# Kernel tuning notes

Measured on AMD Instinct MI355X. Metric: run time of the kernel, lower is better.

Reference implementation:

```python
import jax, jax.numpy as jnp
import numpy as np

N_NODES = 50000
N_EDGES = 800000
D_IN, H, D_OUT = 128, 128, 64


def setup_inputs() -> dict:
    key = jax.random.key(0)
    ks = jax.random.split(key, 8)
    x = jax.random.normal(ks[0], (N_NODES, D_IN), dtype=jnp.float32)
    edge_index = jax.random.randint(ks[1], (2, N_EDGES), 0, N_NODES, dtype=jnp.int64)
    s = 0.05
    return {
        "x": x,
        "edge_index": edge_index,
        # PyG Linear weights are [out, in]; y = x @ W.T + b
        "W_rel1": jax.random.normal(ks[2], (H, D_IN), dtype=jnp.float32) * s,
        "W_root1": jax.random.normal(ks[3], (H, D_IN), dtype=jnp.float32) * s,
        "b1": jax.random.normal(ks[4], (H,), dtype=jnp.float32) * s,
        "W_rel2": jax.random.normal(ks[5], (D_OUT, H), dtype=jnp.float32) * s,
        "W_root2": jax.random.normal(ks[6], (D_OUT, H), dtype=jnp.float32) * s,
        "b2": jax.random.normal(ks[7], (D_OUT,), dtype=jnp.float32) * s,
    }


def graph_conv(x, src, dst, W_rel, W_root, b):
    # sum-aggregate raw neighbor features, then apply linear (equivalent to
    # transforming each message first, but cheaper: one gather + one GEMM).
    agg = jax.ops.segment_sum(x[src], dst, num_segments=N_NODES)  # [N, D]
    return jnp.einsum('nd,hd->nh', agg, W_rel) \
         + jnp.einsum('nd,hd->nh', x, W_root) + b


def reference(x, edge_index, W_rel1, W_root1, b1, W_rel2, W_root2, b2):
    src, dst = edge_index[0], edge_index[1]  # messages flow src -> dst
    t = jax.nn.relu(graph_conv(x, src, dst, W_rel1, W_root1, b1))
    t = graph_conv(t, src, dst, W_rel2, W_root2, b2)
    return t
```

## Files before the change

### kernel.cpp

```cpp
#include <hip/hip_runtime.h>

#define NNODES 50000
#define DIM 128
#define SCAN_CHUNK 4096
#define NSCAN 13
#define PREP_BLOCKS 3200
#define POISON ((int)0xAAAAAAAA)

typedef __attribute__((ext_vector_type(8))) __bf16 bf16x8;
typedef __attribute__((ext_vector_type(4))) float f32x4;

__device__ inline unsigned short f2b(float f) {
    unsigned int u = __float_as_uint(f);
    u += 0x7fffu + ((u >> 16) & 1u);
    return (unsigned short)(u >> 16);
}
__device__ inline float blo(unsigned int u) { return __uint_as_float(u << 16); }
__device__ inline float bhi(unsigned int u) { return __uint_as_float(u & 0xffff0000u); }
__device__ inline unsigned int pack2(float a, float b) {
    return (unsigned int)f2b(a) | ((unsigned int)f2b(b) << 16);
}

__global__ __launch_bounds__(256) void k_prep(
    const float* __restrict__ x, unsigned short* __restrict__ xb, int n4,
    const float* __restrict__ Wa1, const float* __restrict__ Wb1,
    const float* __restrict__ Wa2, const float* __restrict__ Wb2,
    unsigned short* __restrict__ wa1, unsigned short* __restrict__ wb1,
    unsigned short* __restrict__ wa2, unsigned short* __restrict__ wb2,
    const int* __restrict__ dst, int* __restrict__ counts,
    unsigned short* __restrict__ rank, int n_edges)
{
    const int gid = blockIdx.x * 256 + threadIdx.x;

    const int i1 = blockIdx.x * 512 + threadIdx.x;
    const int i2 = i1 + 256;
    const bool ok1 = i1 < n4, ok2 = i2 < n4;
    float4 v1, v2;
    if (ok1) v1 = reinterpret_cast<const float4*>(x)[i1];
    if (ok2) v2 = reinterpret_cast<const float4*>(x)[i2];

    if (gid < n_edges) {
        const int rep = threadIdx.x & 3;
        int rk = atomicAdd(&counts[rep * NNODES + dst[gid]], 1) - POISON;
        rank[gid] = (unsigned short)(rk | (rep << 14));
    }

    if (gid < 16384) { wa1[gid] = f2b(Wa1[gid]); wb1[gid] = f2b(Wb1[gid]); }
    if (gid < 8192)  { wa2[gid] = f2b(Wa2[gid]); wb2[gid] = f2b(Wb2[gid]); }

    if (ok1) {
        uint2 o;
        o.x = pack2(v1.x, v1.y);
        o.y = pack2(v1.z, v1.w);
        reinterpret_cast<uint2*>(xb)[i1] = o;
    }
    if (ok2) {
        uint2 o;
        o.x = pack2(v2.x, v2.y);
        o.y = pack2(v2.z, v2.w);
        reinterpret_cast<uint2*>(xb)[i2] = o;
    }
}

__global__ __launch_bounds__(1024) void k_scan_local(
    const int* __restrict__ counts, int* __restrict__ rowptr,
    int* __restrict__ bsum, uint2* __restrict__ repx2, int n)
{
    __shared__ int wsum[16];
    const int lane = threadIdx.x & 63;
    const int wid = threadIdx.x >> 6;
    int i = blockIdx.x * SCAN_CHUNK + threadIdx.x * 4;
    int4 v = make_int4(0, 0, 0, 0);
    if (i + 3 < n) {
        int4 c0 = *reinterpret_cast<const int4*>(counts + i);
        int4 c1 = *reinterpret_cast<const int4*>(counts + NNODES + i);
        int4 c2 = *reinterpret_cast<const int4*>(counts + 2 * NNODES + i);
        int4 c3 = *reinterpret_cast<const int4*>(counts + 3 * NNODES + i);
        c0.x -= POISON; c0.y -= POISON; c0.z -= POISON; c0.w -= POISON;
        c1.x -= POISON; c1.y -= POISON; c1.z -= POISON; c1.w -= POISON;
        c2.x -= POISON; c2.y -= POISON; c2.z -= POISON; c2.w -= POISON;
        c3.x -= POISON; c3.y -= POISON; c3.z -= POISON; c3.w -= POISON;
        v.x = c0.x + c1.x + c2.x + c3.x;
        v.y = c0.y + c1.y + c2.y + c3.y;
        v.z = c0.z + c1.z + c2.z + c3.z;
        v.w = c0.w + c1.w + c2.w + c3.w;
        uint2 r0, r1g, r2g, r3g;
        r0.x  = (unsigned)(c0.x) << 16;
        r0.y  = (unsigned)(c0.x + c1.x) | ((unsigned)(c0.x + c1.x + c2.x) << 16);
        r1g.x = (unsigned)(c0.y) << 16;
        r1g.y = (unsigned)(c0.y + c1.y) | ((unsigned)(c0.y + c1.y + c2.y) << 16);
        r2g.x = (unsigned)(c0.z) << 16;
        r2g.y = (unsigned)(c0.z + c1.z) | ((unsigned)(c0.z + c1.z + c2.z) << 16);
        r3g.x = (unsigned)(c0.w) << 16;
        r3g.y = (unsigned)(c0.w + c1.w) | ((unsigned)(c0.w + c1.w + c2.w) << 16);
        repx2[i + 0] = r0;
        repx2[i + 1] = r1g;
        repx2[i + 2] = r2g;
        repx2[i + 3] = r3g;
    } else {
#pragma unroll
        for (int j = 0; j < 3; ++j) {
            if (i + j < n) {
                int c0 = counts[i + j] - POISON;
                int c1 = counts[NNODES + i + j] - POISON;
                int c2 = counts[2 * NNODES + i + j] - POISON;
                int c3 = counts[3 * NNODES + i + j] - POISON;
                int t = c0 + c1 + c2 + c3;
                if (j == 0) v.x = t; else if (j == 1) v.y = t; else v.z = t;
                uint2 r;
                r.x = (unsigned)c0 << 16;
                r.y = (unsigned)(c0 + c1) | ((unsigned)(c0 + c1 + c2) << 16);
                repx2[i + j] = r;
            }
        }
    }
    int tot = v.x + v.y + v.z + v.w;
    int s = tot;
#pragma unroll
    for (int off = 1; off < 64; off <<= 1) {
        int t = __shfl_up(s, off);
        if (lane >= off) s += t;
    }
    if (lane == 63) wsum[wid] = s;
    __syncthreads();
    if (wid == 0 && lane < 16) {
        int ws = wsum[lane];
#pragma unroll
        for (int off = 1; off < 16; off <<= 1) {
            int t = __shfl_up(ws, off);
            if (lane >= off) ws += t;
        }
        wsum[lane] = ws;
    }
    __syncthreads();
    int prefix = ((wid > 0) ? wsum[wid - 1] : 0) + (s - tot);
    int4 o;
    o.x = prefix;
    o.y = prefix + v.x;
    o.z = o.y + v.y;
    o.w = o.z + v.z;
    if (i + 3 <= n) {
        *reinterpret_cast<int4*>(rowptr + i) = o;
    } else {
        if (i + 0 <= n) rowptr[i + 0] = o.x;
        if (i + 1 <= n) rowptr[i + 1] = o.y;
        if (i + 2 <= n) rowptr[i + 2] = o.z;
    }
    if (threadIdx.x == 1023) bsum[blockIdx.x] = wsum[15];
}

__device__ inline void build_prefix_lds(const int* __restrict__ bsum, int* pre) {
    if (threadIdx.x < 16) {
        int off = 0;
#pragma unroll 1
        for (int j = 0; j < NSCAN && j < (int)threadIdx.x; ++j) off += bsum[j];
        pre[threadIdx.x] = off;
    }
    __syncthreads();
}

__device__ inline int rep_off(uint2 rp, int r) {
    unsigned pw = (r & 2) ? rp.y : rp.x;
    return (r & 1) ? (int)(pw >> 16) : (int)(pw & 0xffffu);
}

__global__ __launch_bounds__(256) void k_place_gemm1(
    const int* __restrict__ src, const int* __restrict__ dst,
    const unsigned short* __restrict__ rank, const int* __restrict__ rowptr,
    const int* __restrict__ bsum, const uint2* __restrict__ repx2,
    unsigned short* __restrict__ srcs_sorted, int n_edges, int pblocks,
    const unsigned short* __restrict__ A,
    const unsigned short* __restrict__ Wu,
    const unsigned short* __restrict__ Wr,
    const float* __restrict__ bias,
    unsigned short* __restrict__ U,
    unsigned short* __restrict__ R,
    int n_nodes)
{
    if (blockIdx.x < (unsigned)pblocks) {
        __shared__ int pre[16];
        build_prefix_lds(bsum, pre);
        int e = ((int)blockIdx.x * 256 + threadIdx.x) * 8;
        if (e + 7 < n_edges) {
            int4 s4a = *reinterpret_cast<const int4*>(src + e);
            int4 s4b = *reinterpret_cast<const int4*>(src + e + 4);
            int4 d4a = *reinterpret_cast<const int4*>(dst + e);
            int4 d4b = *reinterpret_cast<const int4*>(dst + e + 4);
            uint4 r8 = *reinterpret_cast<const uint4*>(rank + e);
            unsigned rk[8];
            rk[0] = r8.x & 0xffffu; rk[1] = r8.x >> 16;
            rk[2] = r8.y & 0xffffu; rk[3] = r8.y >> 16;
            rk[4] = r8.z & 0xffffu; rk[5] = r8.z >> 16;
            rk[6] = r8.w & 0xffffu; rk[7] = r8.w >> 16;
            int dd[8] = {d4a.x, d4a.y, d4a.z, d4a.w, d4b.x, d4b.y, d4b.z, d4b.w};
            int ss[8] = {s4a.x, s4a.y, s4a.z, s4a.w, s4b.x, s4b.y, s4b.z, s4b.w};
#pragma unroll
            for (int j = 0; j < 8; ++j) {
                const int d = dd[j];
                const int r = (int)(rk[j] >> 14);
                const int rv = (int)(rk[j] & 0x3fffu);
                uint2 rp = repx2[d];
                srcs_sorted[rowptr[d] + pre[d >> 12] + rep_off(rp, r) + rv] =
                    (unsigned short)ss[j];
            }
        } else {
            for (; e < n_edges; ++e) {
                int d = dst[e];
                unsigned rk16 = rank[e];
                int r = (int)(rk16 >> 14);
                int rv = (int)(rk16 & 0x3fffu);
                uint2 rp = repx2[d];
                srcs_sorted[rowptr[d] + pre[d >> 12] + rep_off(rp, r) + rv] =
                    (unsigned short)src[e];
            }
        }
        return;
    }

    constexpr int BN = 128;
    constexpr int NT = BN / 32;
    const int bid = (int)blockIdx.x - pblocks;
    const int tid = threadIdx.x;
    const int wave = tid >> 6;
    const int lane = tid & 63;
    const int quad = lane >> 4;
    const int l16 = lane & 15;
    const int wr = wave >> 1;
    const int wc = wave & 1;
    const int n0 = bid * 32;
    const int node = n0 + wr * 16 + l16;
    const bool ok = node < n_nodes;

    f32x4 accU[NT], accR[NT];
#pragma unroll
    for (int nt = 0; nt < NT; ++nt) {
        f32x4 z = {0.f, 0.f, 0.f, 0.f};
        accU[nt] = z;
        accR[nt] = z;
    }

#pragma unroll 1
    for (int kk = 0; kk < 2; ++kk) {
        const int ko = kk * 64;
        bf16x8 a0 = {}, a1 = {};
        if (ok) {
            a0 = *reinterpret_cast<const bf16x8*>(A + (size_t)node * DIM + ko + quad * 8);
            a1 = *reinterpret_cast<const bf16x8*>(A + (size_t)node * DIM + ko + 32 + quad * 8);
        }
#pragma unroll
        for (int nt = 0; nt < NT; ++nt) {
            const size_t woff = (size_t)(wc * (BN / 2) + nt * 16 + l16) * DIM + ko + quad * 8;
            bf16x8 bu0 = *reinterpret_cast<const bf16x8*>(Wu + woff);
            bf16x8 br0 = *reinterpret_cast<const bf16x8*>(Wr + woff);
            accU[nt] = __builtin_amdgcn_mfma_f32_16x16x32_bf16(bu0, a0, accU[nt], 0, 0, 0);
            accR[nt] = __builtin_amdgcn_mfma_f32_16x16x32_bf16(br0, a0, accR[nt], 0, 0, 0);
            bf16x8 bu1 = *reinterpret_cast<const bf16x8*>(Wu + woff + 32);
            bf16x8 br1 = *reinterpret_cast<const bf16x8*>(Wr + woff + 32);
            accU[nt] = __builtin_amdgcn_mfma_f32_16x16x32_bf16(bu1, a1, accU[nt], 0, 0, 0);
            accR[nt] = __builtin_amdgcn_mfma_f32_16x16x32_bf16(br1, a1, accR[nt], 0, 0, 0);
        }
    }

    if (ok) {
#pragma unroll
        for (int nt = 0; nt < NT; ++nt) {
            const int colb = wc * (BN / 2) + nt * 16 + quad * 4;
            const float4 bv = *reinterpret_cast<const float4*>(bias + colb);
            uint2 uo, ro;
            uo.x = pack2(accU[nt][0], accU[nt][1]);
            uo.y = pack2(accU[nt][2], accU[nt][3]);
            ro.x = pack2(accR[nt][0] + bv.x, accR[nt][1] + bv.y);
            ro.y = pack2(accR[nt][2] + bv.z, accR[nt][3] + bv.w);
            *reinterpret_cast<uint2*>(U + (size_t)node * BN + colb) = uo;
            *reinterpret_cast<uint2*>(R + (size_t)node * BN + colb) = ro;
        }
    }
}

__global__ __launch_bounds__(256) void k_g1_gemm2(
    const unsigned short* __restrict__ U1, const unsigned short* __restrict__ R1,
    const int* __restrict__ rowptr, const int* __restrict__ bsum,
    const unsigned short* __restrict__ srcs,
    const unsigned short* __restrict__ Wu2,
    const unsigned short* __restrict__ Wr2,
    const float* __restrict__ bias2,
    unsigned short* __restrict__ U2,
    unsigned short* __restrict__ R2)
{
    __shared__ int pre[16];
    __shared__ __align__(16) unsigned short tt[16][136];
    build_prefix_lds(bsum, pre);

    const int tid = threadIdx.x;
    const int nl = tid >> 4;
    const int node = blockIdx.x * 16 + nl;
    const int seg = tid & 15;

    {
        int beg = rowptr[node] + pre[node >> 12];
        int end = rowptr[node + 1] + pre[(node + 1) >> 12];
        float acc[8];
#pragma unroll
        for (int i = 0; i < 8; ++i) acc[i] = 0.f;
        int e = beg;
#pragma unroll 1
        for (; e + 7 < end; e += 8) {
            uint4 v[8];
#pragma unroll
            for (int u = 0; u < 8; ++u) {
                int s = srcs[e + u];
                v[u] = *reinterpret_cast<const uint4*>(U1 + (size_t)s * DIM + seg * 8);
            }
#pragma unroll
            for (int u = 0; u < 8; ++u) {
                acc[0] += blo(v[u].x); acc[1] += bhi(v[u].x);
                acc[2] += blo(v[u].y); acc[3] += bhi(v[u].y);
                acc[4] += blo(v[u].z); acc[5] += bhi(v[u].z);
                acc[6] += blo(v[u].w); acc[7] += bhi(v[u].w);
            }
        }
#pragma unroll 1
        for (; e + 1 < end; e += 2) {
            int s0 = srcs[e], s1 = srcs[e + 1];
            uint4 v0 = *reinterpret_cast<const uint4*>(U1 + (size_t)s0 * DIM + seg * 8);
            uint4 v1 = *reinterpret_cast<const uint4*>(U1 + (size_t)s1 * DIM + seg * 8);
            acc[0] += blo(v0.x) + blo(v1.x); acc[1] += bhi(v0.x) + bhi(v1.x);
            acc[2] += blo(v0.y) + blo(v1.y); acc[3] += bhi(v0.y) + bhi(v1.y);
            acc[4] += blo(v0.z) + blo(v1.z); acc[5] += bhi(v0.z) + bhi(v1.z);
            acc[6] += blo(v0.w) + blo(v1.w); acc[7] += bhi(v0.w) + bhi(v1.w);
        }
        if (e < end) {
            int s0 = srcs[e];
            uint4 v = *reinterpret_cast<const uint4*>(U1 + (size_t)s0 * DIM + seg * 8);
            acc[0] += blo(v.x); acc[1] += bhi(v.x);
            acc[2] += blo(v.y); acc[3] += bhi(v.y);
            acc[4] += blo(v.z); acc[5] += bhi(v.z);
            acc[6] += blo(v.w); acc[7] += bhi(v.w);
        }
        uint4 rv = *reinterpret_cast<const uint4*>(R1 + (size_t)node * DIM + seg * 8);
        acc[0] += blo(rv.x); acc[1] += bhi(rv.x);
        acc[2] += blo(rv.y); acc[3] += bhi(rv.y);
        acc[4] += blo(rv.z); acc[5] += bhi(rv.z);
        acc[6] += blo(rv.w); acc[7] += bhi(rv.w);
#pragma unroll
        for (int i = 0; i < 8; ++i) acc[i] = fmaxf(acc[i], 0.f);
        uint4 o;
        o.x = pack2(acc[0], acc[1]);
        o.y = pack2(acc[2], acc[3]);
        o.z = pack2(acc[4], acc[5]);
        o.w = pack2(acc[6], acc[7]);
        *reinterpret_cast<uint4*>(&tt[nl][seg * 8]) = o;
    }
    __syncthreads();

    const int wave = tid >> 6;
    const int lane = tid & 63;
    const int quad = lane >> 4;
    const int l16 = lane & 15;

    f32x4 aU = {0.f, 0.f, 0.f, 0.f};
    f32x4 aR = {0.f, 0.f, 0.f, 0.f};
#pragma unroll
    for (int kk = 0; kk < 4; ++kk) {
        const int ko = kk * 32;
        bf16x8 xf = *reinterpret_cast<const bf16x8*>(&tt[l16][ko + quad * 8]);
        const size_t woff = (size_t)(wave * 16 + l16) * DIM + ko + quad * 8;
        bf16x8 wu = *reinterpret_cast<const bf16x8*>(Wu2 + woff);
        bf16x8 wrg = *reinterpret_cast<const bf16x8*>(Wr2 + woff);
        aU = __builtin_amdgcn_mfma_f32_16x16x32_bf16(wu, xf, aU, 0, 0, 0);
        aR = __builtin_amdgcn_mfma_f32_16x16x32_bf16(wrg, xf, aR, 0, 0, 0);
    }

    const int onode = blockIdx.x * 16 + l16;
    const int colb = wave * 16 + quad * 4;
    const float4 bv = *reinterpret_cast<const float4*>(bias2 + colb);
    uint2 uo, ro;
    uo.x = pack2(aU[0], aU[1]);
    uo.y = pack2(aU[2], aU[3]);
    ro.x = pack2(aR[0] + bv.x, aR[1] + bv.y);
    ro.y = pack2(aR[2] + bv.z, aR[3] + bv.w);
    *reinterpret_cast<uint2*>(U2 + (size_t)onode * 64 + colb) = uo;
    *reinterpret_cast<uint2*>(R2 + (size_t)onode * 64 + colb) = ro;
}

__global__ __launch_bounds__(256) void k_gather_ep2(
    const unsigned short* __restrict__ U, const unsigned short* __restrict__ R,
    const int* __restrict__ rowptr, const int* __restrict__ bsum,
    const unsigned short* __restrict__ srcs, float* __restrict__ out)
{
    __shared__ int pre[16];
    build_prefix_lds(bsum, pre);
    int node = blockIdx.x * 32 + (threadIdx.x >> 3);
    if (node >= NNODES) return;
    int seg = threadIdx.x & 7;
    int beg = rowptr[node] + pre[node >> 12];
    int end = rowptr[node + 1] + pre[(node + 1) >> 12];
    float acc[8];
#pragma unroll
    for (int i = 0; i < 8; ++i) acc[i] = 0.f;
    int e = beg;
#pragma unroll 1
    for (; e + 7 < end; e += 8) {
        uint4 v[8];
#pragma unroll
        for (int u = 0; u < 8; ++u) {
            int s = srcs[e + u];
            v[u] = *reinterpret_cast<const uint4*>(U + (size_t)s * 64 + seg * 8);
        }
#pragma unroll
        for (int u = 0; u < 8; ++u) {
            acc[0] += blo(v[u].x); acc[1] += bhi(v[u].x);
            acc[2] += blo(v[u].y); acc[3] += bhi(v[u].y);
            acc[4] += blo(v[u].z); acc[5] += bhi(v[u].z);
            acc[6] += blo(v[u].w); acc[7] += bhi(v[u].w);
        }
    }
#pragma unroll 1
    for (; e + 1 < end; e += 2) {
        int s0 = srcs[e], s1 = srcs[e + 1];
        uint4 v0 = *reinterpret_cast<const uint4*>(U + (size_t)s0 * 64 + seg * 8);
        uint4 v1 = *reinterpret_cast<const uint4*>(U + (size_t)s1 * 64 + seg * 8);
        acc[0] += blo(v0.x) + blo(v1.x); acc[1] += bhi(v0.x) + bhi(v1.x);
        acc[2] += blo(v0.y) + blo(v1.y); acc[3] += bhi(v0.y) + bhi(v1.y);
        acc[4] += blo(v0.z) + blo(v1.z); acc[5] += bhi(v0.z) + bhi(v1.z);
        acc[6] += blo(v0.w) + blo(v1.w); acc[7] += bhi(v0.w) + bhi(v1.w);
    }
    if (e < end) {
        int s0 = srcs[e];
        uint4 v = *reinterpret_cast<const uint4*>(U + (size_t)s0 * 64 + seg * 8);
        acc[0] += blo(v.x); acc[1] += bhi(v.x);
        acc[2] += blo(v.y); acc[3] += bhi(v.y);
        acc[4] += blo(v.z); acc[5] += bhi(v.z);
        acc[6] += blo(v.w); acc[7] += bhi(v.w);
    }
    uint4 rv = *reinterpret_cast<const uint4*>(R + (size_t)node * 64 + seg * 8);
    acc[0] += blo(rv.x); acc[1] += bhi(rv.x);
    acc[2] += blo(rv.y); acc[3] += bhi(rv.y);
    acc[4] += blo(rv.z); acc[5] += bhi(rv.z);
    acc[6] += blo(rv.w); acc[7] += bhi(rv.w);
    float4 o0 = make_float4(acc[0], acc[1], acc[2], acc[3]);
    float4 o1 = make_float4(acc[4], acc[5], acc[6], acc[7]);
    float* op = out + (size_t)node * 64 + seg * 8;
    *reinterpret_cast<float4*>(op) = o0;
    *reinterpret_cast<float4*>(op + 4) = o1;
}

extern "C" void kernel_launch(void* const* d_in, const int* in_sizes, int n_in,
                              void* d_out, int out_size, void* d_ws, size_t ws_size,
                              hipStream_t stream) {
    const float* x       = (const float*)d_in[0];
    const int*   ei      = (const int*)d_in[1];
    const float* W_rel1  = (const float*)d_in[2];
    const float* W_root1 = (const float*)d_in[3];
    const float* b1      = (const float*)d_in[4];
    const float* W_rel2  = (const float*)d_in[5];
    const float* W_root2 = (const float*)d_in[6];
    const float* b2      = (const float*)d_in[7];

    const int n_edges = in_sizes[1] / 2;
    const int* src = ei;
    const int* dst = ei + n_edges;

    const size_t NELEM = (size_t)NNODES * DIM;
    unsigned short* xb   = (unsigned short*)d_ws;
    unsigned short* u1   = xb + NELEM;
    unsigned short* r1   = u1 + NELEM;
    unsigned short* u2   = r1 + NELEM;
    unsigned short* r2   = u2 + (size_t)NNODES * 64;
    unsigned short* wa1  = r2 + (size_t)NNODES * 64;
    unsigned short* wb1  = wa1 + 16384;
    unsigned short* wa2  = wb1 + 16384;
    unsigned short* wb2  = wa2 + 8192;
    int* counts = (int*)(wb2 + 8192);
    int* rowptr = counts + 4 * NNODES;
    int* bsum   = rowptr + (NNODES + 4);
    uint2* repx2 = (uint2*)(bsum + 20);
    unsigned short* rank16 = (unsigned short*)(repx2 + NNODES);
    unsigned short* srcs16 = rank16 + n_edges;

    float* out = (float*)d_out;

    const int n4 = NNODES * DIM / 4;
    const int pblocks = (n_edges + 2047) / 2048;
    const int gemm_blocks = (NNODES + 31) / 32;
    const int fgblocks = NNODES / 16;
    const int g2blocks = (NNODES + 31) / 32;
    const int sblocks = NSCAN;

    k_prep<<<PREP_BLOCKS, 256, 0, stream>>>(
        x, xb, n4, W_rel1, W_root1, W_rel2, W_root2,
        wa1, wb1, wa2, wb2, dst, counts, rank16, n_edges);

    k_scan_local<<<sblocks, 1024, 0, stream>>>(counts, rowptr, bsum, repx2, NNODES);

    k_place_gemm1<<<pblocks + gemm_blocks, 256, 0, stream>>>(
        src, dst, rank16, rowptr, bsum, repx2, srcs16, n_edges, pblocks,
        xb, wa1, wb1, b1, u1, r1, NNODES);

    k_g1_gemm2<<<fgblocks, 256, 0, stream>>>(
        u1, r1, rowptr, bsum, srcs16, wa2, wb2, b2, u2, r2);

    k_gather_ep2<<<g2blocks, 256, 0, stream>>>(u2, r2, rowptr, bsum, srcs16, out);
}
```

Baseline: 226.2 us.

## Aggregate raw features before layer-1 GEMM and fuse it into gather kernel

Layer 1 no longer precomputes U1/R1 transforms per node. The fused kernel now gathers and sums raw bf16 x rows per destination and stages them with the node's own row in LDS. It then runs both layer-1 GEMMs, bias and ReLU in-block before the layer-2 transform. This removes the 2x128-wide U1/R1 writes and reads and the separate GEMM pass. In exchange each block redoes layer-1 GEMM work for only 16 nodes with weights from global memory, and edge placement becomes its own launch.

```diff
diff --git a/kernel.cpp b/kernel.cpp
--- a/kernel.cpp
+++ b/kernel.cpp
@@ -164,130 +164,66 @@
     return (r & 1) ? (int)(pw >> 16) : (int)(pw & 0xffffu);
 }
 
-__global__ __launch_bounds__(256) void k_place_gemm1(
+__global__ __launch_bounds__(256) void k_place(
     const int* __restrict__ src, const int* __restrict__ dst,
     const unsigned short* __restrict__ rank, const int* __restrict__ rowptr,
     const int* __restrict__ bsum, const uint2* __restrict__ repx2,
-    unsigned short* __restrict__ srcs_sorted, int n_edges, int pblocks,
-    const unsigned short* __restrict__ A,
-    const unsigned short* __restrict__ Wu,
-    const unsigned short* __restrict__ Wr,
-    const float* __restrict__ bias,
-    unsigned short* __restrict__ U,
-    unsigned short* __restrict__ R,
-    int n_nodes)
+    unsigned short* __restrict__ srcs_sorted, int n_edges)
 {
-    if (blockIdx.x < (unsigned)pblocks) {
-        __shared__ int pre[16];
-        build_prefix_lds(bsum, pre);
-        int e = ((int)blockIdx.x * 256 + threadIdx.x) * 8;
-        if (e + 7 < n_edges) {
-            int4 s4a = *reinterpret_cast<const int4*>(src + e);
-            int4 s4b = *reinterpret_cast<const int4*>(src + e + 4);
-            int4 d4a = *reinterpret_cast<const int4*>(dst + e);
-            int4 d4b = *reinterpret_cast<const int4*>(dst + e + 4);
-            uint4 r8 = *reinterpret_cast<const uint4*>(rank + e);
-            unsigned rk[8];
-            rk[0] = r8.x & 0xffffu; rk[1] = r8.x >> 16;
-            rk[2] = r8.y & 0xffffu; rk[3] = r8.y >> 16;
-            rk[4] = r8.z & 0xffffu; rk[5] = r8.z >> 16;
-            rk[6] = r8.w & 0xffffu; rk[7] = r8.w >> 16;
-            int dd[8] = {d4a.x, d4a.y, d4a.z, d4a.w, d4b.x, d4b.y, d4b.z, d4b.w};
-            int ss[8] = {s4a.x, s4a.y, s4a.z, s4a.w, s4b.x, s4b.y, s4b.z, s4b.w};
-#pragma unroll
-            for (int j = 0; j < 8; ++j) {
-                const int d = dd[j];
-                const int r = (int)(rk[j] >> 14);
-                const int rv = (int)(rk[j] & 0x3fffu);
-                uint2 rp = repx2[d];
-                srcs_sorted[rowptr[d] + pre[d >> 12] + rep_off(rp, r) + rv] =
-                    (unsigned short)ss[j];
-            }
-        } else {
-            for (; e < n_edges; ++e) {
-                int d = dst[e];
-                unsigned rk16 = rank[e];
-                int r = (int)(rk16 >> 14);
-                int rv = (int)(rk16 & 0x3fffu);
-                uint2 rp = repx2[d];
-                srcs_sorted[rowptr[d] + pre[d >> 12] + rep_off(rp, r) + rv] =
-                    (unsigned short)src[e];
-            }
-        }
-        return;
-    }
-
-    constexpr int BN = 128;
-    constexpr int NT = BN / 32;
-    const int bid = (int)blockIdx.x - pblocks;
-    const int tid = threadIdx.x;
-    const int wave = tid >> 6;
-    const int lane = tid & 63;
-    const int quad = lane >> 4;
-    const int l16 = lane & 15;
-    const int wr = wave >> 1;
-    const int wc = wave & 1;
-    const int n0 = bid * 32;
-    const int node = n0 + wr * 16 + l16;
-    const bool ok = node < n_nodes;
-
-    f32x4 accU[NT], accR[NT];
-#pragma unroll
-    for (int nt = 0; nt < NT; ++nt) {
-        f32x4 z = {0.f, 0.f, 0.f, 0.f};
-        accU[nt] = z;
-        accR[nt] = z;
-    }
-
-#pragma unroll 1
-    for (int kk = 0; kk < 2; ++kk) {
-        const int ko = kk * 64;
-        bf16x8 a0 = {}, a1 = {};
-        if (ok) {
-            a0 = *reinterpret_cast<const bf16x8*>(A + (size_t)node * DIM + ko + quad * 8);
-            a1 = *reinterpret_cast<const bf16x8*>(A + (size_t)node * DIM + ko + 32 + quad * 8);
-        }
-#pragma unroll
-        for (int nt = 0; nt < NT; ++nt) {
-            const size_t woff = (size_t)(wc * (BN / 2) + nt * 16 + l16) * DIM + ko + quad * 8;
-            bf16x8 bu0 = *reinterpret_cast<const bf16x8*>(Wu + woff);
-            bf16x8 br0 = *reinterpret_cast<const bf16x8*>(Wr + woff);
-            accU[nt] = __builtin_amdgcn_mfma_f32_16x16x32_bf16(bu0, a0, accU[nt], 0, 0, 0);
-            accR[nt] = __builtin_amdgcn_mfma_f32_16x16x32_bf16(br0, a0, accR[nt], 0, 0, 0);
-            bf16x8 bu1 = *reinterpret_cast<const bf16x8*>(Wu + woff + 32);
-            bf16x8 br1 = *reinterpret_cast<const bf16x8*>(Wr + woff + 32);
-            accU[nt] = __builtin_amdgcn_mfma_f32_16x16x32_bf16(bu1, a1, accU[nt], 0, 0, 0);
-            accR[nt] = __builtin_amdgcn_mfma_f32_16x16x32_bf16(br1, a1, accR[nt], 0, 0, 0);
-        }
-    }
-
-    if (ok) {
-#pragma unroll
-        for (int nt = 0; nt < NT; ++nt) {
-            const int colb = wc * (BN / 2) + nt * 16 + quad * 4;
-            const float4 bv = *reinterpret_cast<const float4*>(bias + colb);
-            uint2 uo, ro;
-            uo.x = pack2(accU[nt][0], accU[nt][1]);
-            uo.y = pack2(accU[nt][2], accU[nt][3]);
-            ro.x = pack2(accR[nt][0] + bv.x, accR[nt][1] + bv.y);
-            ro.y = pack2(accR[nt][2] + bv.z, accR[nt][3] + bv.w);
-            *reinterpret_cast<uint2*>(U + (size_t)node * BN + colb) = uo;
-            *reinterpret_cast<uint2*>(R + (size_t)node * BN + colb) = ro;
-        }
-    }
-}
-
-__global__ __launch_bounds__(256) void k_g1_gemm2(
-    const unsigned short* __restrict__ U1, const unsigned short* __restrict__ R1,
+    __shared__ int pre[16];
+    build_prefix_lds(bsum, pre);
+    int e = (blockIdx.x * 256 + threadIdx.x) * 8;
+    if (e + 7 < n_edges) {
+        int4 s4a = *reinterpret_cast<const int4*>(src + e);
+        int4 s4b = *reinterpret_cast<const int4*>(src + e + 4);
+        int4 d4a = *reinterpret_cast<const int4*>(dst + e);
+        int4 d4b = *reinterpret_cast<const int4*>(dst + e + 4);
+        uint4 r8 = *reinterpret_cast<const uint4*>(rank + e);
+        unsigned rk[8];
+        rk[0] = r8.x & 0xffffu; rk[1] = r8.x >> 16;
+        rk[2] = r8.y & 0xffffu; rk[3] = r8.y >> 16;
+        rk[4] = r8.z & 0xffffu; rk[5] = r8.z >> 16;
+        rk[6] = r8.w & 0xffffu; rk[7] = r8.w >> 16;
+        int dd[8] = {d4a.x, d4a.y, d4a.z, d4a.w, d4b.x, d4b.y, d4b.z, d4b.w};
+        int ss[8] = {s4a.x, s4a.y, s4a.z, s4a.w, s4b.x, s4b.y, s4b.z, s4b.w};
+#pragma unroll
+        for (int j = 0; j < 8; ++j) {
+            const int d = dd[j];
+            const int r = (int)(rk[j] >> 14);
+            const int rv = (int)(rk[j] & 0x3fffu);
+            uint2 rp = repx2[d];
+            srcs_sorted[rowptr[d] + pre[d >> 12] + rep_off(rp, r) + rv] =
+                (unsigned short)ss[j];
+        }
+    } else {
+        for (; e < n_edges; ++e) {
+            int d = dst[e];
+            unsigned rk16 = rank[e];
+            int r = (int)(rk16 >> 14);
+            int rv = (int)(rk16 & 0x3fffu);
+            uint2 rp = repx2[d];
+            srcs_sorted[rowptr[d] + pre[d >> 12] + rep_off(rp, r) + rv] =
+                (unsigned short)src[e];
+        }
+    }
+}
+
+__global__ __launch_bounds__(256) void k_fused1(
+    const unsigned short* __restrict__ xb,
     const int* __restrict__ rowptr, const int* __restrict__ bsum,
     const unsigned short* __restrict__ srcs,
-    const unsigned short* __restrict__ Wu2,
+    const unsigned short* __restrict__ Wr1,
+    const unsigned short* __restrict__ Wo1,
+    const float* __restrict__ b1,
     const unsigned short* __restrict__ Wr2,
-    const float* __restrict__ bias2,
+    const unsigned short* __restrict__ Wo2,
+    const float* __restrict__ b2,
     unsigned short* __restrict__ U2,
     unsigned short* __restrict__ R2)
 {
     __shared__ int pre[16];
+    __shared__ __align__(16) unsigned short agg[16][136];
+    __shared__ __align__(16) unsigned short xt[16][136];
     __shared__ __align__(16) unsigned short tt[16][136];
     build_prefix_lds(bsum, pre);
 
@@ -297,6 +233,9 @@
     const int seg = tid & 15;
 
     {
+        *reinterpret_cast<uint4*>(&xt[nl][seg * 8]) =
+            *reinterpret_cast<const uint4*>(xb + (size_t)node * DIM + seg * 8);
+
         int beg = rowptr[node] + pre[node >> 12];
         int end = rowptr[node + 1] + pre[(node + 1) >> 12];
         float acc[8];
@@ -309,7 +248,7 @@
 #pragma unroll
             for (int u = 0; u < 8; ++u) {
                 int s = srcs[e + u];
-                v[u] = *reinterpret_cast<const uint4*>(U1 + (size_t)s * DIM + seg * 8);
+                v[u] = *reinterpret_cast<const uint4*>(xb + (size_t)s * DIM + seg * 8);
             }
 #pragma unroll
             for (int u = 0; u < 8; ++u) {
@@ -322,8 +261,8 @@
 #pragma unroll 1
         for (; e + 1 < end; e += 2) {
             int s0 = srcs[e], s1 = srcs[e + 1];
-            uint4 v0 = *reinterpret_cast<const uint4*>(U1 + (size_t)s0 * DIM + seg * 8);
-            uint4 v1 = *reinterpret_cast<const uint4*>(U1 + (size_t)s1 * DIM + seg * 8);
+            uint4 v0 = *reinterpret_cast<const uint4*>(xb + (size_t)s0 * DIM + seg * 8);
+            uint4 v1 = *reinterpret_cast<const uint4*>(xb + (size_t)s1 * DIM + seg * 8);
             acc[0] += blo(v0.x) + blo(v1.x); acc[1] += bhi(v0.x) + bhi(v1.x);
             acc[2] += blo(v0.y) + blo(v1.y); acc[3] += bhi(v0.y) + bhi(v1.y);
             acc[4] += blo(v0.z) + blo(v1.z); acc[5] += bhi(v0.z) + bhi(v1.z);
@@ -331,25 +270,18 @@
         }
         if (e < end) {
             int s0 = srcs[e];
-            uint4 v = *reinterpret_cast<const uint4*>(U1 + (size_t)s0 * DIM + seg * 8);
+            uint4 v = *reinterpret_cast<const uint4*>(xb + (size_t)s0 * DIM + seg * 8);
             acc[0] += blo(v.x); acc[1] += bhi(v.x);
             acc[2] += blo(v.y); acc[3] += bhi(v.y);
             acc[4] += blo(v.z); acc[5] += bhi(v.z);
             acc[6] += blo(v.w); acc[7] += bhi(v.w);
         }
-        uint4 rv = *reinterpret_cast<const uint4*>(R1 + (size_t)node * DIM + seg * 8);
-        acc[0] += blo(rv.x); acc[1] += bhi(rv.x);
-        acc[2] += blo(rv.y); acc[3] += bhi(rv.y);
-        acc[4] += blo(rv.z); acc[5] += bhi(rv.z);
-        acc[6] += blo(rv.w); acc[7] += bhi(rv.w);
-#pragma unroll
-        for (int i = 0; i < 8; ++i) acc[i] = fmaxf(acc[i], 0.f);
         uint4 o;
         o.x = pack2(acc[0], acc[1]);
         o.y = pack2(acc[2], acc[3]);
         o.z = pack2(acc[4], acc[5]);
         o.w = pack2(acc[6], acc[7]);
-        *reinterpret_cast<uint4*>(&tt[nl][seg * 8]) = o;
+        *reinterpret_cast<uint4*>(&agg[nl][seg * 8]) = o;
     }
     __syncthreads();
 
@@ -358,6 +290,42 @@
     const int quad = lane >> 4;
     const int l16 = lane & 15;
 
+    {
+        f32x4 at0 = {0.f, 0.f, 0.f, 0.f};
+        f32x4 at1 = {0.f, 0.f, 0.f, 0.f};
+#pragma unroll
+        for (int kk = 0; kk < 4; ++kk) {
+            const int ko = kk * 32;
+            bf16x8 af = *reinterpret_cast<const bf16x8*>(&agg[l16][ko + quad * 8]);
+            bf16x8 xf = *reinterpret_cast<const bf16x8*>(&xt[l16][ko + quad * 8]);
+            const size_t w0 = (size_t)(wave * 32 + l16) * DIM + ko + quad * 8;
+            const size_t w1 = w0 + (size_t)16 * DIM;
+            bf16x8 wr0 = *reinterpret_cast<const bf16x8*>(Wr1 + w0);
+            bf16x8 wo0 = *reinterpret_cast<const bf16x8*>(Wo1 + w0);
+            bf16x8 wr1 = *reinterpret_cast<const bf16x8*>(Wr1 + w1);
+            bf16x8 wo1 = *reinterpret_cast<const bf16x8*>(Wo1 + w1);
+            at0 = __builtin_amdgcn_mfma_f32_16x16x32_bf16(wr0, af, at0, 0, 0, 0);
+            at0 = __builtin_amdgcn_mfma_f32_16x16x32_bf16(wo0, xf, at0, 0, 0, 0);
+            at1 = __builtin_amdgcn_mfma_f32_16x16x32_bf16(wr1, af, at1, 0, 0, 0);
+            at1 = __builtin_amdgcn_mfma_f32_16x16x32_bf16(wo1, xf, at1, 0, 0, 0);
+        }
+        {
+            const int colb0 = wave * 32 + quad * 4;
+            const float4 bv0 = *reinterpret_cast<const float4*>(b1 + colb0);
+            uint2 t0;
+            t0.x = pack2(fmaxf(at0[0] + bv0.x, 0.f), fmaxf(at0[1] + bv0.y, 0.f));
+            t0.y = pack2(fmaxf(at0[2] + bv0.z, 0.f), fmaxf(at0[3] + bv0.w, 0.f));
+            *reinterpret_cast<uint2*>(&tt[l16][colb0]) = t0;
+            const int colb1 = colb0 + 16;
+            const float4 bv1 = *reinterpret_cast<const float4*>(b1 + colb1);
+            uint2 t1;
+            t1.x = pack2(fmaxf(at1[0] + bv1.x, 0.f), fmaxf(at1[1] + bv1.y, 0.f));
+            t1.y = pack2(fmaxf(at1[2] + bv1.z, 0.f), fmaxf(at1[3] + bv1.w, 0.f));
+            *reinterpret_cast<uint2*>(&tt[l16][colb1]) = t1;
+        }
+    }
+    __syncthreads();
+
     f32x4 aU = {0.f, 0.f, 0.f, 0.f};
     f32x4 aR = {0.f, 0.f, 0.f, 0.f};
 #pragma unroll
@@ -365,15 +333,14 @@
         const int ko = kk * 32;
         bf16x8 xf = *reinterpret_cast<const bf16x8*>(&tt[l16][ko + quad * 8]);
         const size_t woff = (size_t)(wave * 16 + l16) * DIM + ko + quad * 8;
-        bf16x8 wu = *reinterpret_cast<const bf16x8*>(Wu2 + woff);
-        bf16x8 wrg = *reinterpret_cast<const bf16x8*>(Wr2 + woff);
+        bf16x8 wu = *reinterpret_cast<const bf16x8*>(Wr2 + woff);
+        bf16x8 wrg = *reinterpret_cast<const bf16x8*>(Wo2 + woff);
         aU = __builtin_amdgcn_mfma_f32_16x16x32_bf16(wu, xf, aU, 0, 0, 0);
         aR = __builtin_amdgcn_mfma_f32_16x16x32_bf16(wrg, xf, aR, 0, 0, 0);
     }
-
     const int onode = blockIdx.x * 16 + l16;
     const int colb = wave * 16 + quad * 4;
-    const float4 bv = *reinterpret_cast<const float4*>(bias2 + colb);
+    const float4 bv = *reinterpret_cast<const float4*>(b2 + colb);
     uint2 uo, ro;
     uo.x = pack2(aU[0], aU[1]);
     uo.y = pack2(aU[2], aU[3]);
@@ -463,9 +430,7 @@
 
     const size_t NELEM = (size_t)NNODES * DIM;
     unsigned short* xb   = (unsigned short*)d_ws;
-    unsigned short* u1   = xb + NELEM;
-    unsigned short* r1   = u1 + NELEM;
-    unsigned short* u2   = r1 + NELEM;
+    unsigned short* u2   = xb + NELEM;
     unsigned short* r2   = u2 + (size_t)NNODES * 64;
     unsigned short* wa1  = r2 + (size_t)NNODES * 64;
     unsigned short* wb1  = wa1 + 16384;
@@ -482,8 +447,7 @@
 
     const int n4 = NNODES * DIM / 4;
     const int pblocks = (n_edges + 2047) / 2048;
-    const int gemm_blocks = (NNODES + 31) / 32;
-    const int fgblocks = NNODES / 16;
+    const int f1blocks = NNODES / 16;
     const int g2blocks = (NNODES + 31) / 32;
     const int sblocks = NSCAN;
 
@@ -493,12 +457,11 @@
 
     k_scan_local<<<sblocks, 1024, 0, stream>>>(counts, rowptr, bsum, repx2, NNODES);
 
-    k_place_gemm1<<<pblocks + gemm_blocks, 256, 0, stream>>>(
-        src, dst, rank16, rowptr, bsum, repx2, srcs16, n_edges, pblocks,
-        xb, wa1, wb1, b1, u1, r1, NNODES);
-
-    k_g1_gemm2<<<fgblocks, 256, 0, stream>>>(
-        u1, r1, rowptr, bsum, srcs16, wa2, wb2, b2, u2, r2);
+    k_place<<<pblocks, 256, 0, stream>>>(src, dst, rank16, rowptr, bsum, repx2,
+                                         srcs16, n_edges);
+
+    k_fused1<<<f1blocks, 256, 0, stream>>>(
+        xb, rowptr, bsum, srcs16, wa1, wb1, b1, wa2, wb2, b2, u2, r2);
 
     k_gather_ep2<<<g2blocks, 256, 0, stream>>>(u2, r2, rowptr, bsum, srcs16, out);
 }
```

Measured after the change: 216.2 us. 1.05x faster.
